# Optimization experiments

Hardware: AMD Instinct MI355X
Metric: run time of the kernel (lower is better)

## Reference

```python
import jax, jax.numpy as jnp
import numpy as np

B, C, H, W = 8, 256, 64, 64


def setup_inputs() -> dict:
    key = jax.random.key(0)
    ks = jax.random.split(key, 7)
    s = 1.0 / np.sqrt(C)
    x = jax.random.normal(ks[0], (B, C, H, W), dtype=jnp.float32)
    # 1x1 conv weights collapse to [out_c, in_c] matrices + bias
    wq = jax.random.normal(ks[1], (C, C), dtype=jnp.float32) * s
    bq = jax.random.normal(ks[2], (C,), dtype=jnp.float32) * 0.01
    wk = jax.random.normal(ks[3], (C, C), dtype=jnp.float32) * s
    bk = jax.random.normal(ks[4], (C,), dtype=jnp.float32) * 0.01
    wv = jax.random.normal(ks[5], (C, C), dtype=jnp.float32) * s
    bv = jax.random.normal(ks[6], (C,), dtype=jnp.float32) * 0.01
    return {"x": x, "wq": wq, "bq": bq, "wk": wk, "bk": bk, "wv": wv, "bv": bv}


def reference(x, wq, bq, wk, bk, wv, bv):
    b, c, h, w = x.shape
    n = h * w
    xf = x.reshape(b, c, n)  # [B, C, N]
    # 1x1 convs == per-pixel channel GEMMs
    q = jnp.einsum("oc,bcn->bon", wq, xf) + bq[None, :, None]  # [B, C, N]
    k = jnp.einsum("oc,bcn->bon", wk, xf) + bk[None, :, None]
    v = jnp.einsum("oc,bcn->bon", wv, xf) + bv[None, :, None]
    # scores[b,i,j] = sum_c q[b,c,i] * k[b,c,j]   (no scaling in original)
    scores = jnp.einsum("bci,bcj->bij", q, k)  # [B, N, N]
    attn = jax.nn.softmax(scores, axis=-1)
    # out[b,c,i] = sum_j v[b,c,j] * attn[b,i,j]  (bmm(value, attention^T))
    out = jnp.einsum("bcj,bij->bci", v, attn)
    return out.reshape(b, c, h, w)
```

## Files before the change

### kernel.cpp

```cpp
#include <hip/hip_runtime.h>
#include <hip/hip_bf16.h>


#define BATCH 8
#define CH    256
#define NPIX  4096

typedef unsigned short ushort;
typedef __attribute__((ext_vector_type(8))) short short8;
typedef __attribute__((ext_vector_type(4))) float f32x4;

__device__ __forceinline__ ushort f2bf(float f) {
  unsigned u = __float_as_uint(f);
  unsigned r = (u + 0x7FFFu + ((u >> 16) & 1u)) >> 16;
  return (ushort)r;
}
__device__ __forceinline__ float bf2f(ushort h) {
  return __uint_as_float(((unsigned)h) << 16);
}

__global__ __launch_bounds__(256) void transpose_w(
    const float* __restrict__ wq, const float* __restrict__ wk,
    const float* __restrict__ wv, float* __restrict__ wTq,
    float* __restrict__ wTk, float* __restrict__ wTv) {
  __shared__ float s[64][65];
  const int which = blockIdx.z;
  const float* w = which == 0 ? wq : which == 1 ? wk : wv;
  float* wT      = which == 0 ? wTq : which == 1 ? wTk : wTv;
  const int r0 = blockIdx.x * 64, c0 = blockIdx.y * 64;
  const int t = threadIdx.x;
  for (int idx = t; idx < 4096; idx += 256) {
    int r = idx >> 6, c = idx & 63;
    s[r][c] = w[(r0 + r) * 256 + c0 + c];
  }
  __syncthreads();
  for (int idx = t; idx < 4096; idx += 256) {
    int c = idx >> 6, r = idx & 63;
    wT[(c0 + c) * 256 + r0 + r] = s[r][c];
  }
}

__global__ __launch_bounds__(256) void proj_fused(
    const float* __restrict__ x,
    const float* __restrict__ wTq, const float* __restrict__ bq,
    const float* __restrict__ wTk, const float* __restrict__ bk,
    const float* __restrict__ wTv, const float* __restrict__ bv,
    short* __restrict__ qh, short* __restrict__ ql,
    short* __restrict__ kh, short* __restrict__ kl,
    short* __restrict__ vbuf) {
  __shared__ __align__(16) float xs[64][256];
  const int gid = blockIdx.x;
  const int b = gid >> 6;
  const int ntile = (gid >> 2) & 15;
  const int ob = (gid & 3) * 64;
  const int n0 = ntile * 256;
  const int t = threadIdx.x;

#pragma unroll 1
  for (int pass = 0; pass < 3; ++pass) {
    const float* wT   = pass == 0 ? wTq : pass == 1 ? wTk : wTv;
    const float* bias = pass == 0 ? bq  : pass == 1 ? bk  : bv;
    float acc[64];
#pragma unroll
    for (int o = 0; o < 64; ++o) acc[o] = bias[ob + o];

#pragma unroll 1
    for (int cs = 0; cs < 256; cs += 64) {
      __syncthreads();
      for (int idx = t; idx < 64 * 64; idx += 256) {
        int r = idx >> 6, c4 = idx & 63;
        *(float4*)&xs[r][c4 * 4] =
            *(const float4*)&x[((size_t)b * CH + cs + r) * NPIX + n0 + c4 * 4];
      }
      __syncthreads();
#pragma unroll 2
      for (int cc = 0; cc < 64; ++cc) {
        const float xv = xs[cc][t];
        const float* __restrict__ wrow = wT + (cs + cc) * 256 + ob;
#pragma unroll
        for (int o = 0; o < 64; ++o) acc[o] += wrow[o] * xv;
      }
    }

    if (pass < 2) {
      short* oph = (pass == 0 ? qh : kh) + ((size_t)b * NPIX + n0 + t) * CH + ob;
      short* opl = (pass == 0 ? ql : kl) + ((size_t)b * NPIX + n0 + t) * CH + ob;
#pragma unroll
      for (int g = 0; g < 8; ++g) {
        short8 ph, pl;
#pragma unroll
        for (int e = 0; e < 8; ++e) {
          float vv = acc[g * 8 + e];
          ushort hh = f2bf(vv);
          ph[e] = (short)hh;
          pl[e] = (short)f2bf(vv - bf2f(hh));
        }
        *(short8*)(oph + g * 8) = ph;
        *(short8*)(opl + g * 8) = pl;
      }
    } else {
#pragma unroll 1
      for (int o = 0; o < 64; ++o) {
        vbuf[((size_t)b * CH + ob + o) * NPIX + n0 + t] = (short)f2bf(acc[o]);
      }
    }
  }
}

#define QBLK 64
#define KBLK 32

__global__ __launch_bounds__(256, 2) void attn_kernel(
    const short* __restrict__ qh, const short* __restrict__ ql,
    const short* __restrict__ kh, const short* __restrict__ kl,
    const short* __restrict__ vb, float* __restrict__ out) {
  __shared__ __align__(16) short khs[KBLK * CH];
  __shared__ __align__(16) short kls[KBLK * CH];
  __shared__ __align__(16) short vs[CH][40];
  __shared__ __align__(16) short ps[4][16][40];

  const int phys = blockIdx.x;
  const int lid  = (phys & 7) * 64 + (phys >> 3);
  const int b  = lid >> 6;
  const int i0 = (lid & 63) * QBLK;

  const int tid = threadIdx.x;
  const int w = tid >> 6, l = tid & 63;
  const int l15 = l & 15, q4 = l >> 4;
  const int cbase = q4 * 8;

  short8 qfh[8], qfl[8];
  {
    const size_t qrow = (size_t)b * NPIX + i0 + w * 16 + l15;
    const short* ph = qh + qrow * CH + cbase;
    const short* pl = ql + qrow * CH + cbase;
#pragma unroll
    for (int kc = 0; kc < 8; ++kc) {
      qfh[kc] = *(const short8*)(ph + kc * 32);
      qfl[kc] = *(const short8*)(pl + kc * 32);
    }
  }

  f32x4 o[16];
#pragma unroll
  for (int i = 0; i < 16; ++i) o[i] = (f32x4){0.f, 0.f, 0.f, 0.f};
  f32x4 o_l = (f32x4){0.f, 0.f, 0.f, 0.f};
  float m_r[4] = {-1e30f, -1e30f, -1e30f, -1e30f};

  const short8 onesf = (short8){0x3F80, 0x3F80, 0x3F80, 0x3F80,
                                0x3F80, 0x3F80, 0x3F80, 0x3F80};

  const int krow = w * 8 + (l & 7);
  const int kcb  = l >> 3;
  const short* gkh = kh + (size_t)b * NPIX * CH;
  const short* gkl = kl + (size_t)b * NPIX * CH;
  const short* gv  = vb + (size_t)b * CH * NPIX;

  short8 rkh[4], rkl[4], rv[4];
#pragma unroll
  for (int s = 0; s < 4; ++s) {
    const size_t ko = (size_t)krow * CH + (size_t)(kcb + 8 * s) * 8;
    rkh[s] = *(const short8*)(gkh + ko);
    rkl[s] = *(const short8*)(gkl + ko);
    rv[s]  = *(const short8*)(gv + (size_t)(s * 64 + w * 16 + (l >> 2)) * NPIX + (l & 3) * 8);
  }

#pragma unroll 1
  for (int j0 = 0; j0 < NPIX; j0 += KBLK) {
    __syncthreads();
#pragma unroll
    for (int s = 0; s < 4; ++s) {
      int wb = (krow * 512 + (kcb + 8 * s) * 16) ^ ((krow & 7) << 4);
      *(short8*)((char*)khs + wb) = rkh[s];
      *(short8*)((char*)kls + wb) = rkl[s];
      *(short8*)&vs[s * 64 + w * 16 + (l >> 2)][(l & 3) * 8] = rv[s];
    }
    __syncthreads();

    const int jn = j0 + KBLK;
    if (jn < NPIX) {
#pragma unroll
      for (int s = 0; s < 4; ++s) {
        const size_t ko = (size_t)(jn + krow) * CH + (size_t)(kcb + 8 * s) * 8;
        rkh[s] = *(const short8*)(gkh + ko);
        rkl[s] = *(const short8*)(gkl + ko);
        rv[s]  = *(const short8*)(gv + (size_t)(s * 64 + w * 16 + (l >> 2)) * NPIX + jn + (l & 3) * 8);
      }
    }

    f32x4 sa[2][2];
    sa[0][0] = (f32x4){0.f, 0.f, 0.f, 0.f};
    sa[0][1] = (f32x4){0.f, 0.f, 0.f, 0.f};
    sa[1][0] = (f32x4){0.f, 0.f, 0.f, 0.f};
    sa[1][1] = (f32x4){0.f, 0.f, 0.f, 0.f};
#pragma unroll
    for (int kc = 0; kc < 8; ++kc) {
      const int h = kc >> 2;
      int byte0 = (l15 * 512 + (kc * 32 + cbase) * 2) ^ ((l15 & 7) << 4);
      int byte1 = ((l15 + 16) * 512 + (kc * 32 + cbase) * 2) ^ ((l15 & 7) << 4);
      short8 bh0 = *(const short8*)((const char*)khs + byte0);
      short8 bh1 = *(const short8*)((const char*)khs + byte1);
      short8 bl0 = *(const short8*)((const char*)kls + byte0);
      short8 bl1 = *(const short8*)((const char*)kls + byte1);
      sa[h][0] = __builtin_amdgcn_mfma_f32_16x16x32_bf16(qfh[kc], bh0, sa[h][0], 0, 0, 0);
      sa[h][1] = __builtin_amdgcn_mfma_f32_16x16x32_bf16(qfh[kc], bh1, sa[h][1], 0, 0, 0);
      sa[h][0] = __builtin_amdgcn_mfma_f32_16x16x32_bf16(qfl[kc], bh0, sa[h][0], 0, 0, 0);
      sa[h][1] = __builtin_amdgcn_mfma_f32_16x16x32_bf16(qfl[kc], bh1, sa[h][1], 0, 0, 0);
      sa[h][0] = __builtin_amdgcn_mfma_f32_16x16x32_bf16(qfh[kc], bl0, sa[h][0], 0, 0, 0);
      sa[h][1] = __builtin_amdgcn_mfma_f32_16x16x32_bf16(qfh[kc], bl1, sa[h][1], 0, 0, 0);
    }
    f32x4 s0, s1;
#pragma unroll
    for (int r = 0; r < 4; ++r) { s0[r] = sa[0][0][r] + sa[1][0][r]; s1[r] = sa[0][1][r] + sa[1][1][r]; }

    float scale[4], p0[4], p1[4];
#pragma unroll
    for (int r = 0; r < 4; ++r) {
      float tm = fmaxf(s0[r], s1[r]);
      tm = fmaxf(tm, __shfl_xor(tm, 1));
      tm = fmaxf(tm, __shfl_xor(tm, 2));
      tm = fmaxf(tm, __shfl_xor(tm, 4));
      tm = fmaxf(tm, __shfl_xor(tm, 8));
      if (tm > m_r[r] + 8.f) {
        scale[r] = __expf(m_r[r] - tm);
        m_r[r] = tm;
      } else {
        scale[r] = 1.f;
      }
      p0[r] = __expf(s0[r] - m_r[r]);
      p1[r] = __expf(s1[r] - m_r[r]);
    }
    if (scale[0] != 1.f || scale[1] != 1.f || scale[2] != 1.f || scale[3] != 1.f) {
#pragma unroll
      for (int nt = 0; nt < 16; ++nt) {
        o[nt][0] *= scale[0];
        o[nt][1] *= scale[1];
        o[nt][2] *= scale[2];
        o[nt][3] *= scale[3];
      }
      o_l[0] *= scale[0]; o_l[1] *= scale[1];
      o_l[2] *= scale[2]; o_l[3] *= scale[3];
    }

#pragma unroll
    for (int r = 0; r < 4; ++r) {
      ps[w][q4 * 4 + r][l15]      = (short)f2bf(p0[r]);
      ps[w][q4 * 4 + r][l15 + 16] = (short)f2bf(p1[r]);
    }
    short8 pa = *(const short8*)&ps[w][l15][cbase];
    o_l = __builtin_amdgcn_mfma_f32_16x16x32_bf16(pa, onesf, o_l, 0, 0, 0);
#pragma unroll
    for (int nt = 0; nt < 16; ++nt) {
      short8 vv = *(const short8*)&vs[nt * 16 + l15][cbase];
      o[nt] = __builtin_amdgcn_mfma_f32_16x16x32_bf16(pa, vv, o[nt], 0, 0, 0);
    }
  }

  float inv[4];
#pragma unroll
  for (int r = 0; r < 4; ++r) inv[r] = 1.f / o_l[r];
  float* ob = out + (size_t)b * CH * NPIX + i0 + w * 16;
#pragma unroll
  for (int nt = 0; nt < 16; ++nt) {
    const int c = nt * 16 + l15;
#pragma unroll
    for (int r = 0; r < 4; ++r)
      ob[(size_t)c * NPIX + q4 * 4 + r] = o[nt][r] * inv[r];
  }
}

extern "C" void kernel_launch(void* const* d_in, const int* in_sizes, int n_in,
                              void* d_out, int out_size, void* d_ws, size_t ws_size,
                              hipStream_t stream) {
  const float* x  = (const float*)d_in[0];
  const float* wq = (const float*)d_in[1];
  const float* bq = (const float*)d_in[2];
  const float* wk = (const float*)d_in[3];
  const float* bk = (const float*)d_in[4];
  const float* wv = (const float*)d_in[5];
  const float* bv = (const float*)d_in[6];
  float* out = (float*)d_out;

  const size_t per = (size_t)BATCH * NPIX * CH;
  short* qh = (short*)d_ws;
  short* ql = qh + per;
  short* kh = ql + per;
  short* kl = kh + per;
  short* vb = kl + per;
  float* wTq = (float*)(vb + per);
  float* wTk = wTq + 256 * 256;
  float* wTv = wTk + 256 * 256;

  transpose_w<<<dim3(4, 4, 3), 256, 0, stream>>>(wq, wk, wv, wTq, wTk, wTv);
  proj_fused<<<512, 256, 0, stream>>>(x, wTq, bq, wTk, bk, wTv, bv,
                                      qh, ql, kh, kl, vb);
  attn_kernel<<<512, 256, 0, stream>>>(qh, ql, kh, kl, vb, out);
}
```

Before: 826.8 us.

## Switch to fp16 MFMA projections, drop K low part, async LDS double-buffer attention

```diff
diff --git a/kernel.cpp b/kernel.cpp
--- a/kernel.cpp
+++ b/kernel.cpp
@@ -1,108 +1,198 @@
 #include <hip/hip_runtime.h>
 #include <hip/hip_bf16.h>
+#include <hip/hip_fp16.h>
 
 
 #define BATCH 8
 #define CH    256
 #define NPIX  4096
 
-typedef unsigned short ushort;
-typedef __attribute__((ext_vector_type(8))) short short8;
-typedef __attribute__((ext_vector_type(4))) float f32x4;
-
-__device__ __forceinline__ ushort f2bf(float f) {
-  unsigned u = __float_as_uint(f);
-  unsigned r = (u + 0x7FFFu + ((u >> 16) & 1u)) >> 16;
-  return (ushort)r;
-}
-__device__ __forceinline__ float bf2f(ushort h) {
-  return __uint_as_float(((unsigned)h) << 16);
-}
-
-__global__ __launch_bounds__(256) void transpose_w(
+typedef __attribute__((ext_vector_type(8))) short    short8;
+typedef __attribute__((ext_vector_type(8))) _Float16 half8;
+typedef __attribute__((ext_vector_type(4))) float    f32x4;
+
+__device__ __forceinline__ short f2h_s(float v) {
+  _Float16 h = (_Float16)v;
+  return __builtin_bit_cast(short, h);
+}
+
+__device__ __forceinline__ void gload16(const void* g, void* lds) {
+  __builtin_amdgcn_global_load_lds(
+      (const __attribute__((address_space(1))) unsigned int*)g,
+      (__attribute__((address_space(3))) unsigned int*)lds, 16, 0, 0);
+}
+
+__global__ __launch_bounds__(256) void prep_whl(
     const float* __restrict__ wq, const float* __restrict__ wk,
-    const float* __restrict__ wv, float* __restrict__ wTq,
-    float* __restrict__ wTk, float* __restrict__ wTv) {
-  __shared__ float s[64][65];
-  const int which = blockIdx.z;
-  const float* w = which == 0 ? wq : which == 1 ? wk : wv;
-  float* wT      = which == 0 ? wTq : which == 1 ? wTk : wTv;
-  const int r0 = blockIdx.x * 64, c0 = blockIdx.y * 64;
+    const float* __restrict__ wv, short* __restrict__ whl) {
+  const int m = blockIdx.x >> 8;
+  const int o = blockIdx.x & 255;
+  const float* w = m == 0 ? wq : m == 1 ? wk : wv;
   const int t = threadIdx.x;
-  for (int idx = t; idx < 4096; idx += 256) {
-    int r = idx >> 6, c = idx & 63;
-    s[r][c] = w[(r0 + r) * 256 + c0 + c];
+  float v = w[o * 256 + t];
+  _Float16 h = (_Float16)v;
+  _Float16 lo = (_Float16)(v - (float)h);
+  short* dst = whl + ((size_t)m * 256 + o) * 512;
+  dst[t] = __builtin_bit_cast(short, h);
+  dst[256 + t] = __builtin_bit_cast(short, lo);
+}
+
+__global__ __launch_bounds__(256) void transpose_x(
+    const float* __restrict__ x, short* __restrict__ xT) {
+  __shared__ float tile[64][68];
+  const int id = blockIdx.x;
+  const int b = id >> 8;
+  const int r = id & 255;
+  const int n0 = (r >> 2) * 64, c0 = (r & 3) * 64;
+  const int t = threadIdx.x;
+  const float* xb = x + (size_t)b * CH * NPIX;
+#pragma unroll
+  for (int pass = 0; pass < 4; ++pass) {
+    int c = pass * 16 + (t >> 4);
+    float4 v = *(const float4*)&xb[(size_t)(c0 + c) * NPIX + n0 + (t & 15) * 4];
+    *(float4*)&tile[c][(t & 15) * 4] = v;
   }
   __syncthreads();
-  for (int idx = t; idx < 4096; idx += 256) {
-    int c = idx >> 6, r = idx & 63;
-    wT[(c0 + c) * 256 + r0 + r] = s[r][c];
-  }
-}
-
-__global__ __launch_bounds__(256) void proj_fused(
-    const float* __restrict__ x,
-    const float* __restrict__ wTq, const float* __restrict__ bq,
-    const float* __restrict__ wTk, const float* __restrict__ bk,
-    const float* __restrict__ wTv, const float* __restrict__ bv,
+  const int px = t >> 2;
+#pragma unroll
+  for (int mi = 0; mi < 2; ++mi) {
+    int m = (t & 3) + mi * 4;
+    short8 hh;
+#pragma unroll
+    for (int e = 0; e < 8; ++e) hh[e] = f2h_s(tile[m * 8 + e][px]);
+    *(short8*)&xT[((size_t)b * NPIX + n0 + px) * CH + c0 + m * 8] = hh;
+  }
+}
+
+__global__ __launch_bounds__(256) void proj_gemm(
+    const short* __restrict__ xT, const short* __restrict__ whl,
+    const float* __restrict__ bq, const float* __restrict__ bk,
+    const float* __restrict__ bv,
     short* __restrict__ qh, short* __restrict__ ql,
-    short* __restrict__ kh, short* __restrict__ kl,
-    short* __restrict__ vbuf) {
-  __shared__ __align__(16) float xs[64][256];
-  const int gid = blockIdx.x;
-  const int b = gid >> 6;
-  const int ntile = (gid >> 2) & 15;
-  const int ob = (gid & 3) * 64;
-  const int n0 = ntile * 256;
+    short* __restrict__ kh, short* __restrict__ vbuf) {
+  __shared__ __align__(16) short smem[4 * 8192];
+
+  const int id = blockIdx.x;
+  const int b = id / 192;
+  const int r = id % 192;
+  const int which = r >> 6;
+  const int r2 = r & 63;
+  const int px0 = (r2 >> 1) * 128, o0 = (r2 & 1) * 128;
   const int t = threadIdx.x;
+  const int w = t >> 6, l = t & 63;
+  const int l15 = l & 15, q4 = l >> 4;
+
+  const short* Asrc = xT + ((size_t)b * NPIX + px0) * CH;
+  const short* Bsrc = whl + ((size_t)which * 256 + o0) * 512;
+
+  const int srow = t >> 1;
+  const int scb = (t & 1) * 4;
+
+  f32x4 acc[2][8];
+#pragma unroll
+  for (int i = 0; i < 2; ++i)
+#pragma unroll
+    for (int j = 0; j < 8; ++j) acc[i][j] = (f32x4){0.f, 0.f, 0.f, 0.f};
+
+  short8 ra[4], rb[4];
+#pragma unroll
+  for (int i = 0; i < 4; ++i) {
+    int c = scb + i;
+    ra[i] = *(const short8*)&Asrc[(size_t)srow * CH + 0 + c * 8];
+    rb[i] = *(const short8*)&Bsrc[(size_t)srow * 512 + 0 + c * 8];
+  }
 
 #pragma unroll 1
-  for (int pass = 0; pass < 3; ++pass) {
-    const float* wT   = pass == 0 ? wTq : pass == 1 ? wTk : wTv;
-    const float* bias = pass == 0 ? bq  : pass == 1 ? bk  : bv;
-    float acc[64];
-#pragma unroll
-    for (int o = 0; o < 64; ++o) acc[o] = bias[ob + o];
-
-#pragma unroll 1
-    for (int cs = 0; cs < 256; cs += 64) {
-      __syncthreads();
-      for (int idx = t; idx < 64 * 64; idx += 256) {
-        int r = idx >> 6, c4 = idx & 63;
-        *(float4*)&xs[r][c4 * 4] =
-            *(const float4*)&x[((size_t)b * CH + cs + r) * NPIX + n0 + c4 * 4];
-      }
-      __syncthreads();
-#pragma unroll 2
-      for (int cc = 0; cc < 64; ++cc) {
-        const float xv = xs[cc][t];
-        const float* __restrict__ wrow = wT + (cs + cc) * 256 + ob;
-#pragma unroll
-        for (int o = 0; o < 64; ++o) acc[o] += wrow[o] * xv;
-      }
-    }
-
-    if (pass < 2) {
-      short* oph = (pass == 0 ? qh : kh) + ((size_t)b * NPIX + n0 + t) * CH + ob;
-      short* opl = (pass == 0 ? ql : kl) + ((size_t)b * NPIX + n0 + t) * CH + ob;
-#pragma unroll
-      for (int g = 0; g < 8; ++g) {
-        short8 ph, pl;
-#pragma unroll
-        for (int e = 0; e < 8; ++e) {
-          float vv = acc[g * 8 + e];
-          ushort hh = f2bf(vv);
-          ph[e] = (short)hh;
-          pl[e] = (short)f2bf(vv - bf2f(hh));
+  for (int s = 0; s < 8; ++s) {
+    const int cur = s & 1;
+    short* Asb = smem + cur * 8192;
+    short* Bsb = smem + 16384 + cur * 8192;
+#pragma unroll
+    for (int i = 0; i < 4; ++i) {
+      int c = scb + i;
+      int wb = srow * 128 + ((c ^ (srow & 7)) * 16);
+      *(short8*)((char*)Asb + wb) = ra[i];
+      *(short8*)((char*)Bsb + wb) = rb[i];
+    }
+    __syncthreads();
+    if (s < 7) {
+      int sn = s + 1;
+      const short* Ap = Asrc + (sn & 3) * 64;
+      const short* Bp = Bsrc + sn * 64;
+#pragma unroll
+      for (int i = 0; i < 4; ++i) {
+        int c = scb + i;
+        ra[i] = *(const short8*)&Ap[(size_t)srow * CH + c * 8];
+        rb[i] = *(const short8*)&Bp[(size_t)srow * 512 + c * 8];
+      }
+    }
+#pragma unroll
+    for (int kk = 0; kk < 2; ++kk) {
+      half8 a[2];
+#pragma unroll
+      for (int mb = 0; mb < 2; ++mb) {
+        int row = w * 32 + mb * 16 + l15;
+        int byte = row * 128 + (((kk * 4 + q4) ^ (l15 & 7)) * 16);
+        a[mb] = *(const half8*)((const char*)Asb + byte);
+      }
+#pragma unroll
+      for (int nb = 0; nb < 8; ++nb) {
+        int row = nb * 16 + l15;
+        int byte = row * 128 + (((kk * 4 + q4) ^ (l15 & 7)) * 16);
+        half8 bf = *(const half8*)((const char*)Bsb + byte);
+        acc[0][nb] = __builtin_amdgcn_mfma_f32_16x16x32_f16(a[0], bf, acc[0][nb], 0, 0, 0);
+        acc[1][nb] = __builtin_amdgcn_mfma_f32_16x16x32_f16(a[1], bf, acc[1][nb], 0, 0, 0);
+      }
+    }
+    __syncthreads();
+  }
+
+  const float* bias = which == 0 ? bq : which == 1 ? bk : bv;
+  if (which < 2) {
+#pragma unroll
+    for (int nb = 0; nb < 8; ++nb) {
+      float bv_ = bias[o0 + nb * 16 + l15];
+      int o = o0 + nb * 16 + l15;
+#pragma unroll
+      for (int mb = 0; mb < 2; ++mb) {
+#pragma unroll
+        for (int rr = 0; rr < 4; ++rr) {
+          float v = acc[mb][nb][rr] + bv_;
+          int px = px0 + w * 32 + mb * 16 + q4 * 4 + rr;
+          size_t off = ((size_t)b * NPIX + px) * CH + o;
+          _Float16 h = (_Float16)v;
+          if (which == 0) {
+            qh[off] = __builtin_bit_cast(short, h);
+            ql[off] = f2h_s(v - (float)h);
+          } else {
+            kh[off] = __builtin_bit_cast(short, h);
+          }
         }
-        *(short8*)(oph + g * 8) = ph;
-        *(short8*)(opl + g * 8) = pl;
-      }
-    } else {
-#pragma unroll 1
-      for (int o = 0; o < 64; ++o) {
-        vbuf[((size_t)b * CH + ob + o) * NPIX + n0 + t] = (short)f2bf(acc[o]);
-      }
+      }
+    }
+  } else {
+    short* lt = smem;
+    __syncthreads();
+#pragma unroll
+    for (int nb = 0; nb < 8; ++nb) {
+      float bv_ = bias[o0 + nb * 16 + l15];
+      int o = nb * 16 + l15;
+#pragma unroll
+      for (int mb = 0; mb < 2; ++mb) {
+#pragma unroll
+        for (int rr = 0; rr < 4; ++rr) {
+          int px = w * 32 + mb * 16 + q4 * 4 + rr;
+          lt[o * 136 + px] = f2h_s(acc[mb][nb][rr] + bv_);
+        }
+      }
+    }
+    __syncthreads();
+    const int ot = t >> 1;
+#pragma unroll
+    for (int i = 0; i < 8; ++i) {
+      int c = (t & 1) * 8 + i;
+      short8 vv = *(const short8*)&lt[ot * 136 + c * 8];
+      *(short8*)&vbuf[((size_t)b * CH + o0 + ot) * NPIX + px0 + c * 8] = vv;
     }
   }
 }
@@ -110,13 +200,12 @@
 #define QBLK 64
 #define KBLK 32
 
-__global__ __launch_bounds__(256, 2) void attn_kernel(
+__global__ __launch_bounds__(256) void attn_kernel(
     const short* __restrict__ qh, const short* __restrict__ ql,
-    const short* __restrict__ kh, const short* __restrict__ kl,
-    const short* __restrict__ vb, float* __restrict__ out) {
-  __shared__ __align__(16) short khs[KBLK * CH];
-  __shared__ __align__(16) short kls[KBLK * CH];
-  __shared__ __align__(16) short vs[CH][40];
+    const short* __restrict__ kh, const short* __restrict__ vb,
+    float* __restrict__ out) {
+  __shared__ __align__(16) short khs[2][KBLK * CH];
+  __shared__ __align__(16) short vs[2][CH * KBLK];
   __shared__ __align__(16) short ps[4][16][40];
 
   const int phys = blockIdx.x;
@@ -124,20 +213,19 @@
   const int b  = lid >> 6;
   const int i0 = (lid & 63) * QBLK;
 
-  const int tid = threadIdx.x;
-  const int w = tid >> 6, l = tid & 63;
-  const int l15 = l & 15, q4 = l >> 4;
-  const int cbase = q4 * 8;
-
-  short8 qfh[8], qfl[8];
+  const int t = threadIdx.x;
+  const int w = t >> 6, l = t & 63;
+  const int l15 = l & 15, q4 = l >> 4, cbase = q4 * 8;
+
+  half8 qfh[8], qfl[8];
   {
     const size_t qrow = (size_t)b * NPIX + i0 + w * 16 + l15;
     const short* ph = qh + qrow * CH + cbase;
     const short* pl = ql + qrow * CH + cbase;
 #pragma unroll
     for (int kc = 0; kc < 8; ++kc) {
-      qfh[kc] = *(const short8*)(ph + kc * 32);
-      qfl[kc] = *(const short8*)(pl + kc * 32);
+      qfh[kc] = *(const half8*)(ph + kc * 32);
+      qfl[kc] = *(const half8*)(pl + kc * 32);
     }
   }
 
@@ -147,125 +235,103 @@
   f32x4 o_l = (f32x4){0.f, 0.f, 0.f, 0.f};
   float m_r[4] = {-1e30f, -1e30f, -1e30f, -1e30f};
 
-  const short8 onesf = (short8){0x3F80, 0x3F80, 0x3F80, 0x3F80,
-                                0x3F80, 0x3F80, 0x3F80, 0x3F80};
-
-  const int krow = w * 8 + (l & 7);
-  const int kcb  = l >> 3;
-  const short* gkh = kh + (size_t)b * NPIX * CH;
-  const short* gkl = kl + (size_t)b * NPIX * CH;
-  const short* gv  = vb + (size_t)b * CH * NPIX;
-
-  short8 rkh[4], rkl[4], rv[4];
-#pragma unroll
-  for (int s = 0; s < 4; ++s) {
-    const size_t ko = (size_t)krow * CH + (size_t)(kcb + 8 * s) * 8;
-    rkh[s] = *(const short8*)(gkh + ko);
-    rkl[s] = *(const short8*)(gkl + ko);
-    rv[s]  = *(const short8*)(gv + (size_t)(s * 64 + w * 16 + (l >> 2)) * NPIX + (l & 3) * 8);
-  }
+  half8 onesh;
+#pragma unroll
+  for (int e = 0; e < 8; ++e) onesh[e] = (_Float16)1.0f;
+
+  const short* gk = kh + (size_t)b * NPIX * CH;
+  const short* gv = vb + (size_t)b * CH * NPIX;
+
+  auto issue = [&](int j0, int bn) {
+#pragma unroll
+    for (int i = 0; i < 4; ++i) {
+      const int ins = w * 4 + i;
+      const int krow = ins * 2 + (l >> 5);
+      const int kch = (l & 31) ^ (krow & 7);
+      gload16(gk + ((size_t)(j0 + krow)) * CH + kch * 8,
+              (short*)&khs[bn][0] + ins * 512);
+      const int vch = ins * 16 + (l >> 2);
+      gload16(gv + (size_t)vch * NPIX + j0 + (l & 3) * 8,
+              (short*)&vs[bn][0] + ins * 512);
+    }
+  };
+
+  issue(0, 0);
 
 #pragma unroll 1
   for (int j0 = 0; j0 < NPIX; j0 += KBLK) {
-    __syncthreads();
-#pragma unroll
-    for (int s = 0; s < 4; ++s) {
-      int wb = (krow * 512 + (kcb + 8 * s) * 16) ^ ((krow & 7) << 4);
-      *(short8*)((char*)khs + wb) = rkh[s];
-      *(short8*)((char*)kls + wb) = rkl[s];
-      *(short8*)&vs[s * 64 + w * 16 + (l >> 2)][(l & 3) * 8] = rv[s];
-    }
-    __syncthreads();
-
-    const int jn = j0 + KBLK;
-    if (jn < NPIX) {
-#pragma unroll
-      for (int s = 0; s < 4; ++s) {
-        const size_t ko = (size_t)(jn + krow) * CH + (size_t)(kcb + 8 * s) * 8;
-        rkh[s] = *(const short8*)(gkh + ko);
-        rkl[s] = *(const short8*)(gkl + ko);
-        rv[s]  = *(const short8*)(gv + (size_t)(s * 64 + w * 16 + (l >> 2)) * NPIX + jn + (l & 3) * 8);
-      }
-    }
-
-    f32x4 sa[2][2];
-    sa[0][0] = (f32x4){0.f, 0.f, 0.f, 0.f};
-    sa[0][1] = (f32x4){0.f, 0.f, 0.f, 0.f};
-    sa[1][0] = (f32x4){0.f, 0.f, 0.f, 0.f};
-    sa[1][1] = (f32x4){0.f, 0.f, 0.f, 0.f};
+    const int cur = (j0 >> 5) & 1;
+    asm volatile("s_waitcnt vmcnt(0)" ::: "memory");
+    __syncthreads();
+    if (j0 + KBLK < NPIX) issue(j0 + KBLK, cur ^ 1);
+
+    f32x4 s0h = (f32x4){0.f, 0.f, 0.f, 0.f}, s0l = s0h, s1h = s0h, s1l = s0h;
 #pragma unroll
     for (int kc = 0; kc < 8; ++kc) {
-      const int h = kc >> 2;
       int byte0 = (l15 * 512 + (kc * 32 + cbase) * 2) ^ ((l15 & 7) << 4);
       int byte1 = ((l15 + 16) * 512 + (kc * 32 + cbase) * 2) ^ ((l15 & 7) << 4);
-      short8 bh0 = *(const short8*)((const char*)khs + byte0);
-      short8 bh1 = *(const short8*)((const char*)khs + byte1);
-      short8 bl0 = *(const short8*)((const char*)kls + byte0);
-      short8 bl1 = *(const short8*)((const char*)kls + byte1);
-      sa[h][0] = __builtin_amdgcn_mfma_f32_16x16x32_bf16(qfh[kc], bh0, sa[h][0], 0, 0, 0);
-      sa[h][1] = __builtin_amdgcn_mfma_f32_16x16x32_bf16(qfh[kc], bh1, sa[h][1], 0, 0, 0);
-      sa[h][0] = __builtin_amdgcn_mfma_f32_16x16x32_bf16(qfl[kc], bh0, sa[h][0], 0, 0, 0);
-      sa[h][1] = __builtin_amdgcn_mfma_f32_16x16x32_bf16(qfl[kc], bh1, sa[h][1], 0, 0, 0);
-      sa[h][0] = __builtin_amdgcn_mfma_f32_16x16x32_bf16(qfh[kc], bl0, sa[h][0], 0, 0, 0);
-      sa[h][1] = __builtin_amdgcn_mfma_f32_16x16x32_bf16(qfh[kc], bl1, sa[h][1], 0, 0, 0);
+      half8 b0 = *(const half8*)((const char*)&khs[cur][0] + byte0);
+      half8 b1 = *(const half8*)((const char*)&khs[cur][0] + byte1);
+      s0h = __builtin_amdgcn_mfma_f32_16x16x32_f16(qfh[kc], b0, s0h, 0, 0, 0);
+      s0l = __builtin_amdgcn_mfma_f32_16x16x32_f16(qfl[kc], b0, s0l, 0, 0, 0);
+      s1h = __builtin_amdgcn_mfma_f32_16x16x32_f16(qfh[kc], b1, s1h, 0, 0, 0);
+      s1l = __builtin_amdgcn_mfma_f32_16x16x32_f16(qfl[kc], b1, s1l, 0, 0, 0);
     }
     f32x4 s0, s1;
 #pragma unroll
-    for (int r = 0; r < 4; ++r) { s0[r] = sa[0][0][r] + sa[1][0][r]; s1[r] = sa[0][1][r] + sa[1][1][r]; }
+    for (int rr = 0; rr < 4; ++rr) { s0[rr] = s0h[rr] + s0l[rr]; s1[rr] = s1h[rr] + s1l[rr]; }
 
     float scale[4], p0[4], p1[4];
 #pragma unroll
-    for (int r = 0; r < 4; ++r) {
-      float tm = fmaxf(s0[r], s1[r]);
+    for (int rr = 0; rr < 4; ++rr) {
+      float tm = fmaxf(s0[rr], s1[rr]);
       tm = fmaxf(tm, __shfl_xor(tm, 1));
       tm = fmaxf(tm, __shfl_xor(tm, 2));
       tm = fmaxf(tm, __shfl_xor(tm, 4));
       tm = fmaxf(tm, __shfl_xor(tm, 8));
-      if (tm > m_r[r] + 8.f) {
-        scale[r] = __expf(m_r[r] - tm);
-        m_r[r] = tm;
+      if (tm > m_r[rr] + 8.f) {
+        scale[rr] = __expf(m_r[rr] - tm);
+        m_r[rr] = tm;
       } else {
-        scale[r] = 1.f;
-      }
-      p0[r] = __expf(s0[r] - m_r[r]);
-      p1[r] = __expf(s1[r] - m_r[r]);
+        scale[rr] = 1.f;
+      }
+      p0[rr] = __expf(s0[rr] - m_r[rr]);
+      p1[rr] = __expf(s1[rr] - m_r[rr]);
     }
     if (scale[0] != 1.f || scale[1] != 1.f || scale[2] != 1.f || scale[3] != 1.f) {
 #pragma unroll
       for (int nt = 0; nt < 16; ++nt) {
-        o[nt][0] *= scale[0];
-        o[nt][1] *= scale[1];
-        o[nt][2] *= scale[2];
-        o[nt][3] *= scale[3];
+        o[nt][0] *= scale[0]; o[nt][1] *= scale[1];
+        o[nt][2] *= scale[2]; o[nt][3] *= scale[3];
       }
       o_l[0] *= scale[0]; o_l[1] *= scale[1];
       o_l[2] *= scale[2]; o_l[3] *= scale[3];
     }
 
 #pragma unroll
-    for (int r = 0; r < 4; ++r) {
-      ps[w][q4 * 4 + r][l15]      = (short)f2bf(p0[r]);
-      ps[w][q4 * 4 + r][l15 + 16] = (short)f2bf(p1[r]);
-    }
-    short8 pa = *(const short8*)&ps[w][l15][cbase];
-    o_l = __builtin_amdgcn_mfma_f32_16x16x32_bf16(pa, onesf, o_l, 0, 0, 0);
+    for (int rr = 0; rr < 4; ++rr) {
+      ps[w][q4 * 4 + rr][l15]      = f2h_s(p0[rr]);
+      ps[w][q4 * 4 + rr][l15 + 16] = f2h_s(p1[rr]);
+    }
+    half8 pa = *(const half8*)&ps[w][l15][cbase];
+    o_l = __builtin_amdgcn_mfma_f32_16x16x32_f16(pa, onesh, o_l, 0, 0, 0);
 #pragma unroll
     for (int nt = 0; nt < 16; ++nt) {
-      short8 vv = *(const short8*)&vs[nt * 16 + l15][cbase];
-      o[nt] = __builtin_amdgcn_mfma_f32_16x16x32_bf16(pa, vv, o[nt], 0, 0, 0);
+      half8 vv = *(const half8*)((const short*)&vs[cur][0] + (nt * 16 + l15) * 32 + cbase);
+      o[nt] = __builtin_amdgcn_mfma_f32_16x16x32_f16(pa, vv, o[nt], 0, 0, 0);
     }
   }
 
   float inv[4];
 #pragma unroll
-  for (int r = 0; r < 4; ++r) inv[r] = 1.f / o_l[r];
+  for (int rr = 0; rr < 4; ++rr) inv[rr] = 1.f / o_l[rr];
   float* ob = out + (size_t)b * CH * NPIX + i0 + w * 16;
 #pragma unroll
   for (int nt = 0; nt < 16; ++nt) {
     const int c = nt * 16 + l15;
 #pragma unroll
-    for (int r = 0; r < 4; ++r)
-      ob[(size_t)c * NPIX + q4 * 4 + r] = o[nt][r] * inv[r];
+    for (int rr = 0; rr < 4; ++rr)
+      ob[(size_t)c * NPIX + q4 * 4 + rr] = o[nt][rr] * inv[rr];
   }
 }
 
@@ -282,17 +348,15 @@
   float* out = (float*)d_out;
 
   const size_t per = (size_t)BATCH * NPIX * CH;
-  short* qh = (short*)d_ws;
-  short* ql = qh + per;
-  short* kh = ql + per;
-  short* kl = kh + per;
-  short* vb = kl + per;
-  float* wTq = (float*)(vb + per);
-  float* wTk = wTq + 256 * 256;
-  float* wTv = wTk + 256 * 256;
-
-  transpose_w<<<dim3(4, 4, 3), 256, 0, stream>>>(wq, wk, wv, wTq, wTk, wTv);
-  proj_fused<<<512, 256, 0, stream>>>(x, wTq, bq, wTk, bk, wTv, bv,
-                                      qh, ql, kh, kl, vb);
-  attn_kernel<<<512, 256, 0, stream>>>(qh, ql, kh, kl, vb, out);
-}
+  short* xT  = (short*)d_ws;
+  short* qhb = xT + per;
+  short* qlb = qhb + per;
+  short* khb = qlb + per;
+  short* vbf = khb + per;
+  short* whl = vbf + per;
+
+  prep_whl<<<768, 256, 0, stream>>>(wq, wk, wv, whl);
+  transpose_x<<<2048, 256, 0, stream>>>(x, xT);
+  proj_gemm<<<1536, 256, 0, stream>>>(xT, whl, bq, bk, bv, qhb, qlb, khb, vbf);
+  attn_kernel<<<512, 256, 0, stream>>>(qhb, qlb, khb, vbf, out);
+}
```

Result: faster. 680.1 us (-17.7%).
